# Optimization experiments

Measured on AMD Instinct MI355X. Metric: run time of the kernel, lower is better.

Reference implementation:

```python
import jax, jax.numpy as jnp
import numpy as np

NUM_GROUPS = 32
EPS = 1e-5


def group_norm(x, weight, bias):
    # x: [B, C, H, W]; normalize per (group, sample) over channels-in-group and spatial dims
    B, C, H, W = x.shape
    g = x.reshape(B, NUM_GROUPS, C // NUM_GROUPS, H, W)
    mean = g.mean(axis=(2, 3, 4), keepdims=True)
    var = g.var(axis=(2, 3, 4), keepdims=True)
    g = (g - mean) * jax.lax.rsqrt(var + EPS)
    g = g.reshape(B, C, H, W)
    return g * weight[None, :, None, None] + bias[None, :, None, None]


def conv1x1(x, w, b):
    # x: [B, C, H, W], w: [O, C] (1x1 conv kernel squeezed), b: [O]
    return jnp.einsum('bchw,oc->bohw', x, w) + b[None, :, None, None]


def setup_inputs() -> dict:
    key = jax.random.key(0)
    ks = jax.random.split(key, 6)
    B, C, H, W = 16, 512, 64, 64
    scale = 1.0 / np.sqrt(C)
    x = jax.random.normal(ks[0], (B, C, H, W), dtype=jnp.float32)
    return {
        'x': x,
        'gn_weight': jnp.ones((C,), jnp.float32),
        'gn_bias': jnp.zeros((C,), jnp.float32),
        'wq': jax.random.normal(ks[1], (C, C), jnp.float32) * scale,
        'bq': jnp.zeros((C,), jnp.float32),
        'wk': jax.random.normal(ks[2], (C, C), jnp.float32) * scale,
        'bk': jnp.zeros((C,), jnp.float32),
        'wv': jax.random.normal(ks[3], (C, C), jnp.float32) * scale,
        'bv': jnp.zeros((C,), jnp.float32),
        'wo': jax.random.normal(ks[4], (C, C), jnp.float32) * (scale * 1e-5),
        'bo': jnp.zeros((C,), jnp.float32),
    }


def reference(x, gn_weight, gn_bias, wq, bq, wk, bk, wv, bv, wo, bo):
    B, C, H, W = x.shape
    h = group_norm(x, gn_weight, gn_bias)
    q = conv1x1(h, wq, bq)  # [B, C, H, W]
    k = conv1x1(h, wk, bk)
    v = conv1x1(h, wv, bv)
    q = q.transpose(0, 2, 3, 1).reshape(B, H * W, C)   # [B, HW, C]
    kf = k.reshape(B, C, H * W)                        # [B, C, HW]
    w = jnp.einsum('bnc,bcm->bnm', q, kf) * (C ** -0.5)  # [B, HW, HW]
    w = jax.nn.softmax(w, axis=-1)
    vf = v.transpose(0, 2, 3, 1).reshape(B, H * W, C)
    h = jnp.einsum('bnm,bmc->bnc', w, vf)              # [B, HW, C]
    h = h.reshape(B, H, W, C).transpose(0, 3, 1, 2)    # [B, C, H, W]
    h = conv1x1(h, wo, bo)
    return x + h
```

## Files before the change

### kernel.cpp

```cpp
#include <hip/hip_runtime.h>
#include <stdint.h>

typedef __bf16 bf16x8 __attribute__((ext_vector_type(8)));
typedef float  f32x4  __attribute__((ext_vector_type(4)));
typedef unsigned short ushortx8 __attribute__((ext_vector_type(8)));
typedef unsigned short ushortx4 __attribute__((ext_vector_type(4)));

#define DEVI __device__ __forceinline__

DEVI unsigned short f2bf(float f) {
  union { float f; unsigned int u; } v; v.f = f;
  unsigned int r = v.u + 0x7fffu + ((v.u >> 16) & 1u);
  return (unsigned short)(r >> 16);
}
DEVI float bf2f(unsigned short h) {
  union { unsigned int u; float f; } v; v.u = ((unsigned int)h) << 16;
  return v.f;
}

DEVI void gl_lds16(const unsigned short* g, unsigned short* l) {
  __builtin_amdgcn_global_load_lds(
      (__attribute__((address_space(1))) unsigned int*)g,
      (__attribute__((address_space(3))) unsigned int*)l,
      16, 0, 0);
}

DEVI void raw_barrier() {
  __builtin_amdgcn_sched_barrier(0);
  __builtin_amdgcn_s_barrier();
  __builtin_amdgcn_sched_barrier(0);
}
DEVI void wait_vm4()   { __builtin_amdgcn_s_waitcnt(0x0F74); __builtin_amdgcn_sched_barrier(0); }
DEVI void wait_vm0()   { __builtin_amdgcn_s_waitcnt(0x0F70); __builtin_amdgcn_sched_barrier(0); }
DEVI void wait_lgkm0() { __builtin_amdgcn_s_waitcnt(0xC07F); __builtin_amdgcn_sched_barrier(0); }

DEVI void store_out(float* p, float v) { *p = v; }
DEVI void store_out(unsigned short* p, float v) { *p = f2bf(v); }

__global__ __launch_bounds__(256) void gn_stats(const float* __restrict__ x,
                                                float* __restrict__ stats) {
  const int bg = blockIdx.x;
  const float* p = x + (size_t)bg * 65536;
  const int tid = threadIdx.x;
  float s = 0.f, ss = 0.f;
#pragma unroll 4
  for (int i = 0; i < 64; ++i) {
    float4 v = *(const float4*)(p + (((size_t)i * 256 + tid) << 2));
    s  += v.x + v.y + v.z + v.w;
    ss += v.x * v.x + v.y * v.y + v.z * v.z + v.w * v.w;
  }
  for (int off = 32; off; off >>= 1) { s += __shfl_xor(s, off); ss += __shfl_xor(ss, off); }
  __shared__ float rs[4], rss[4];
  const int lane = tid & 63, wave = tid >> 6;
  if (lane == 0) { rs[wave] = s; rss[wave] = ss; }
  __syncthreads();
  if (tid == 0) {
    float S1 = rs[0] + rs[1] + rs[2] + rs[3];
    float S2 = rss[0] + rss[1] + rss[2] + rss[3];
    float mean = S1 * (1.f / 65536.f);
    float var  = S2 * (1.f / 65536.f) - mean * mean;
    stats[bg * 2 + 0] = mean;
    stats[bg * 2 + 1] = rsqrtf(var + 1e-5f);
  }
}

__global__ __launch_bounds__(256) void gn_apply(const float* __restrict__ x,
                                                const float* __restrict__ stats,
                                                const float* __restrict__ gamma,
                                                const float* __restrict__ beta,
                                                unsigned short* __restrict__ h_t) {
  __shared__ alignas(16) unsigned short tile[64 * 136];
  const int tid = threadIdx.x;
  const int t0 = blockIdx.x * 64;
  const int c0 = blockIdx.y * 128;
  const int b  = blockIdx.z;
  const float* xb = x + ((size_t)b * 512 + c0) * 4096 + t0;
#pragma unroll
  for (int j = 0; j < 8; ++j) {
    int f = tid + j * 256;
    int r = f >> 4;
    int tc = (f & 15) << 2;
    float4 v = *(const float4*)(xb + (size_t)r * 4096 + tc);
    int ch = c0 + r;
    int g = ch >> 4;
    float mean = stats[((size_t)b * 32 + g) * 2 + 0];
    float rstd = stats[((size_t)b * 32 + g) * 2 + 1];
    float ga = gamma[ch] * rstd;
    float be = beta[ch] - mean * ga;
    tile[(tc + 0) * 136 + r] = f2bf(v.x * ga + be);
    tile[(tc + 1) * 136 + r] = f2bf(v.y * ga + be);
    tile[(tc + 2) * 136 + r] = f2bf(v.z * ga + be);
    tile[(tc + 3) * 136 + r] = f2bf(v.w * ga + be);
  }
  __syncthreads();
  unsigned short* hb = h_t + (size_t)b * 4096 * 512;
#pragma unroll
  for (int j = 0; j < 4; ++j) {
    int f = tid + j * 256;
    int tok = f >> 4;
    int cc = (f & 15) << 3;
    ushortx8 v = *(const ushortx8*)&tile[tok * 136 + cc];
    *(ushortx8*)(hb + (size_t)(t0 + tok) * 512 + c0 + cc) = v;
  }
}

__global__ __launch_bounds__(256) void cvt_f32_bf16(const float* __restrict__ s,
                                                    unsigned short* __restrict__ d) {
  int i = (blockIdx.x * 256 + threadIdx.x) * 4;
  float4 v = *(const float4*)(s + i);
  ushortx4 o;
  o[0] = f2bf(v.x); o[1] = f2bf(v.y); o[2] = f2bf(v.z); o[3] = f2bf(v.w);
  *(ushortx4*)(d + i) = o;
}

template <int BIAS_MODE, int RESID, typename OT>
__global__ __launch_bounds__(512, 2) void gemm_nt_256(
    const unsigned short* __restrict__ A, const unsigned short* __restrict__ B,
    OT* __restrict__ D, const float* __restrict__ bias,
    const float* __restrict__ resid, int M, int N, int K,
    long long sA, long long sB, long long sD, long long sR, float alpha) {
  __shared__ alignas(128) char sm[131072];
  char* const sA0 = sm;
  char* const sB0 = sm + 32768;
  char* const sA1 = sm + 65536;
  char* const sB1 = sm + 98304;

  const int tid = threadIdx.x;
  const int bz = blockIdx.x, bn = blockIdx.y, bm = blockIdx.z;
  const unsigned short* Ab = A + (size_t)bz * sA + (size_t)bm * 256 * K;
  const unsigned short* Bb = B + (size_t)bz * sB + (size_t)bn * 256 * K;

  const int lane = tid & 63;
  const int ln = lane & 15, quad = lane >> 4;
  const int wave = tid >> 6;
  const int wm = wave >> 2, wn = wave & 3;

  const int prow = tid >> 3;
  const unsigned ks = (unsigned)((tid & 7) ^ (prow & 7));
  const unsigned srcoff = (unsigned)prow * (unsigned)K + ks * 8u;
  const unsigned ldst = (unsigned)tid * 16u;

  const int aro = (wm * 128 + ln) * 128;
  const int bro = (wn * 64 + ln) * 128;
  const int sl0 = ((quad ^ (ln & 7)) << 4);
  const int sl1 = (((4 + quad) ^ (ln & 7)) << 4);

  f32x4 acc[8][4] = {};
  bf16x8 a0[8], a1[8], b0[4], b1[4];

#define STAGE(G, SMp, h, ktv) do {                                                   \
    const unsigned short* _g = (G) + (unsigned)(h) * 128u * (unsigned)K +            \
                               (unsigned)(ktv) * 64u + srcoff;                       \
    gl_lds16(_g, (unsigned short*)((SMp) + (h) * 16384 + ldst));                     \
    gl_lds16(_g + (size_t)64 * K, (unsigned short*)((SMp) + (h) * 16384 + 8192 + ldst)); \
  } while (0)

#define RD_A(SMp, SL, dst) do { _Pragma("unroll")                                    \
    for (int _mf = 0; _mf < 8; ++_mf)                                                \
      dst[_mf] = *(const bf16x8*)((SMp) + aro + _mf * 2048 + (SL)); } while (0)
#define RD_B(SMp, SL, dst) do { _Pragma("unroll")                                    \
    for (int _nf = 0; _nf < 4; ++_nf)                                                \
      dst[_nf] = *(const bf16x8*)((SMp) + bro + _nf * 2048 + (SL)); } while (0)

#define MM(AF, BF, N0) do {                                                          \
    __builtin_amdgcn_s_setprio(1);                                                   \
    _Pragma("unroll")                                                                \
    for (int _mf = 0; _mf < 8; ++_mf) {                                              \
      acc[_mf][(N0)]     = __builtin_amdgcn_mfma_f32_16x16x32_bf16(AF[_mf], BF[(N0)],     acc[_mf][(N0)],     0, 0, 0); \
      acc[_mf][(N0) + 1] = __builtin_amdgcn_mfma_f32_16x16x32_bf16(AF[_mf], BF[(N0) + 1], acc[_mf][(N0) + 1], 0, 0, 0); \
    }                                                                                \
    __builtin_amdgcn_s_setprio(0);                                                   \
  } while (0)

  STAGE(Ab, sA0, 0, 0); STAGE(Ab, sA0, 1, 0);
  STAGE(Bb, sB0, 0, 0); STAGE(Bb, sB0, 1, 0);
  STAGE(Ab, sA1, 0, 1); STAGE(Ab, sA1, 1, 1);
  wait_vm4();
  raw_barrier();

  const int NI = K >> 7;
  int kt0 = 0;
  for (int i = 0; i < NI - 1; ++i, kt0 += 2) {
    RD_A(sA0, sl0, a0); RD_B(sB0, sl0, b0);
    STAGE(Bb, sB1, 0, kt0 + 1);
    raw_barrier();
    MM(a0, b0, 0);
    raw_barrier();
    RD_A(sA0, sl1, a1); RD_B(sB0, sl1, b1);
    STAGE(Bb, sB1, 1, kt0 + 1);
    raw_barrier();
    MM(a0, b0, 2);
    wait_lgkm0();
    raw_barrier();
    STAGE(Ab, sA0, 0, kt0 + 2);
    raw_barrier();
    MM(a1, b1, 0);
    raw_barrier();
    STAGE(Ab, sA0, 1, kt0 + 2);
    raw_barrier();
    MM(a1, b1, 2);
    wait_vm4();
    raw_barrier();
    RD_A(sA1, sl0, a0); RD_B(sB1, sl0, b0);
    STAGE(Bb, sB0, 0, kt0 + 2);
    raw_barrier();
    MM(a0, b0, 0);
    raw_barrier();
    RD_A(sA1, sl1, a1); RD_B(sB1, sl1, b1);
    STAGE(Bb, sB0, 1, kt0 + 2);
    raw_barrier();
    MM(a0, b0, 2);
    wait_lgkm0();
    raw_barrier();
    STAGE(Ab, sA1, 0, kt0 + 3);
    raw_barrier();
    MM(a1, b1, 0);
    raw_barrier();
    STAGE(Ab, sA1, 1, kt0 + 3);
    raw_barrier();
    MM(a1, b1, 2);
    wait_vm4();
    raw_barrier();
  }
  {
    RD_A(sA0, sl0, a0); RD_B(sB0, sl0, b0);
    STAGE(Bb, sB1, 0, kt0 + 1);
    raw_barrier();
    MM(a0, b0, 0);
    raw_barrier();
    RD_A(sA0, sl1, a1); RD_B(sB0, sl1, b1);
    STAGE(Bb, sB1, 1, kt0 + 1);
    raw_barrier();
    MM(a0, b0, 2);
    MM(a1, b1, 0);
    MM(a1, b1, 2);
    wait_vm0();
    raw_barrier();
    RD_A(sA1, sl0, a0); RD_B(sB1, sl0, b0);
    RD_A(sA1, sl1, a1); RD_B(sB1, sl1, b1);
    MM(a0, b0, 0);
    MM(a0, b0, 2);
    MM(a1, b1, 0);
    MM(a1, b1, 2);
  }
#undef STAGE
#undef RD_A
#undef RD_B
#undef MM

  OT* Db = D + (size_t)bz * sD;
  const float* Rb = RESID ? (resid + (size_t)bz * sR) : nullptr;
#pragma unroll
  for (int mf = 0; mf < 8; ++mf) {
#pragma unroll
    for (int nf = 0; nf < 4; ++nf) {
#pragma unroll
      for (int r = 0; r < 4; ++r) {
        int row = bm * 256 + wm * 128 + mf * 16 + quad * 4 + r;
        int col = bn * 256 + wn * 64 + nf * 16 + ln;
        float v = acc[mf][nf][r] * alpha;
        if (BIAS_MODE == 1) v += bias[row];
        if (BIAS_MODE == 2) v += bias[col];
        size_t idx = (size_t)row * N + col;
        if (RESID) v += Rb[idx];
        store_out(&Db[idx], v);
      }
    }
  }
}

__global__ __launch_bounds__(256) void softmax_rows(unsigned short* __restrict__ S) {
  const int tid = threadIdx.x;
  unsigned short* p = S + (size_t)blockIdx.x * 4096 + tid * 16;
  ushortx8 u0 = *(const ushortx8*)p;
  ushortx8 u1 = *(const ushortx8*)(p + 8);
  float v[16];
#pragma unroll
  for (int i = 0; i < 8; ++i) { v[i] = bf2f(u0[i]); v[i + 8] = bf2f(u1[i]); }
  float m = v[0];
#pragma unroll
  for (int i = 1; i < 16; ++i) m = fmaxf(m, v[i]);
  for (int off = 32; off; off >>= 1) m = fmaxf(m, __shfl_xor(m, off));
  __shared__ float red[4];
  __shared__ float red2[4];
  const int lane = tid & 63, wave = tid >> 6;
  if (lane == 0) red[wave] = m;
  __syncthreads();
  m = fmaxf(fmaxf(red[0], red[1]), fmaxf(red[2], red[3]));
  float s = 0.f;
#pragma unroll
  for (int i = 0; i < 16; ++i) { v[i] = __expf(v[i] - m); s += v[i]; }
  for (int off = 32; off; off >>= 1) s += __shfl_xor(s, off);
  if (lane == 0) red2[wave] = s;
  __syncthreads();
  s = red2[0] + red2[1] + red2[2] + red2[3];
  float inv = 1.f / s;
#pragma unroll
  for (int i = 0; i < 8; ++i) { u0[i] = f2bf(v[i] * inv); u1[i] = f2bf(v[i + 8] * inv); }
  *(ushortx8*)p = u0;
  *(ushortx8*)(p + 8) = u1;
}

extern "C" void kernel_launch(void* const* d_in, const int* in_sizes, int n_in,
                              void* d_out, int out_size, void* d_ws, size_t ws_size,
                              hipStream_t stream) {
  const float* x   = (const float*)d_in[0];
  const float* gnw = (const float*)d_in[1];
  const float* gnb = (const float*)d_in[2];
  const float* wq  = (const float*)d_in[3];
  const float* bq  = (const float*)d_in[4];
  const float* wk  = (const float*)d_in[5];
  const float* bk  = (const float*)d_in[6];
  const float* wv  = (const float*)d_in[7];
  const float* bv  = (const float*)d_in[8];
  const float* wo  = (const float*)d_in[9];
  const float* bo  = (const float*)d_in[10];
  float* out = (float*)d_out;

  const size_t EB = 2097152;

  char* base = (char*)d_ws;
  unsigned short* h_t  = (unsigned short*)base;
  unsigned short* wqb  = (unsigned short*)(base + 67108864);
  unsigned short* wkb  = wqb + 262144;
  unsigned short* wvb  = wkb + 262144;
  unsigned short* wob  = wvb + 262144;
  float*          stats = (float*)(base + 69206016);
  char*           dyn   = base + 69210112;
  size_t rem = ws_size > 69210112 ? ws_size - 69210112 : 0;

  int nb = 1;
  if      (rem >= (size_t)16 * 46137344) nb = 16;
  else if (rem >= (size_t)8  * 46137344) nb = 8;
  else if (rem >= (size_t)4  * 46137344) nb = 4;
  else if (rem >= (size_t)2  * 46137344) nb = 2;

  unsigned short* q  = (unsigned short*)dyn;
  unsigned short* kb = q  + (size_t)nb * EB;
  unsigned short* vb = kb + (size_t)nb * EB;
  unsigned short* Sb = (unsigned short*)(dyn + (size_t)nb * 3 * 4194304);
  unsigned short* attn = q;

  gn_stats<<<512, 256, 0, stream>>>(x, stats);
  gn_apply<<<dim3(64, 4, 16), 256, 0, stream>>>(x, stats, gnw, gnb, h_t);
  cvt_f32_bf16<<<256, 256, 0, stream>>>(wq, wqb);
  cvt_f32_bf16<<<256, 256, 0, stream>>>(wk, wkb);
  cvt_f32_bf16<<<256, 256, 0, stream>>>(wv, wvb);
  cvt_f32_bf16<<<256, 256, 0, stream>>>(wo, wob);

  const float sm_scale = 0.044194173824159216f;

  for (int b0 = 0; b0 < 16; b0 += nb) {
    const unsigned short* hc = h_t + (size_t)b0 * EB;
    gemm_nt_256<2, 0, unsigned short><<<dim3(nb, 2, 16), 512, 0, stream>>>(
        hc, wqb, q, bq, nullptr, 4096, 512, 512, (long long)EB, 0, (long long)EB, 0, 1.f);
    gemm_nt_256<2, 0, unsigned short><<<dim3(nb, 2, 16), 512, 0, stream>>>(
        hc, wkb, kb, bk, nullptr, 4096, 512, 512, (long long)EB, 0, (long long)EB, 0, 1.f);
    gemm_nt_256<1, 0, unsigned short><<<dim3(nb, 16, 2), 512, 0, stream>>>(
        wvb, hc, vb, bv, nullptr, 512, 4096, 512, 0, (long long)EB, (long long)EB, 0, 1.f);
    gemm_nt_256<0, 0, unsigned short><<<dim3(nb, 16, 16), 512, 0, stream>>>(
        q, kb, Sb, nullptr, nullptr, 4096, 4096, 512,
        (long long)EB, (long long)EB, 16777216LL, 0, sm_scale);
    softmax_rows<<<nb * 4096, 256, 0, stream>>>(Sb);
    gemm_nt_256<0, 0, unsigned short><<<dim3(nb, 2, 16), 512, 0, stream>>>(
        Sb, vb, attn, nullptr, nullptr, 4096, 512, 4096,
        16777216LL, (long long)EB, (long long)EB, 0, 1.f);
    gemm_nt_256<1, 1, float><<<dim3(nb, 16, 2), 512, 0, stream>>>(
        wob, attn, out + (size_t)b0 * EB, bo, x + (size_t)b0 * EB,
        512, 4096, 512, 0, (long long)EB, (long long)EB, (long long)EB, 1.f);
  }
}
```

Baseline: 1.242 ms.

## Rewrite GEMM main loop with inline-asm LDS reads and finer waitcnt pipelining

Restructures the bf16 MFMA GEMM main loop so LDS fragment reads for the next sub-step are issued before the current MFMA block, with partial lgkmcnt/vmcnt waits written in inline assembly instead of full drains. Precomputed LDS byte addresses and ds_read_b128 with immediate offsets replace compiler-generated reads, and the staging order is changed so B tiles for two k-steps are prefetched first. The loop now runs uniformly over all iterations, clamping out-of-range tile indices, which removes the separate epilogue but issues redundant loads at the tail. This tries to hide LDS and global latency behind MFMA work. The risk is that hand-set wait counts and asm volatile ordering can be wrong or hamper compiler scheduling.

New measurement: 1.524 ms. 22.7% more time.

```diff
diff --git a/kernel.cpp b/kernel.cpp
--- a/kernel.cpp
+++ b/kernel.cpp
@@ -25,14 +25,17 @@
       16, 0, 0);
 }
 
-DEVI void raw_barrier() {
+DEVI unsigned lds_off(const void* p) {
+  return (unsigned)(unsigned long long)(__attribute__((address_space(3))) const char*)(const char*)p;
+}
+
+DEVI void abar() {
   __builtin_amdgcn_sched_barrier(0);
-  __builtin_amdgcn_s_barrier();
+  asm volatile("s_barrier");
   __builtin_amdgcn_sched_barrier(0);
 }
-DEVI void wait_vm4()   { __builtin_amdgcn_s_waitcnt(0x0F74); __builtin_amdgcn_sched_barrier(0); }
-DEVI void wait_vm0()   { __builtin_amdgcn_s_waitcnt(0x0F70); __builtin_amdgcn_sched_barrier(0); }
-DEVI void wait_lgkm0() { __builtin_amdgcn_s_waitcnt(0xC07F); __builtin_amdgcn_sched_barrier(0); }
+#define AWT_VM(N)   do { asm volatile("s_waitcnt vmcnt(" #N ")");   __builtin_amdgcn_sched_barrier(0); } while (0)
+#define AWT_LGKM(N) do { asm volatile("s_waitcnt lgkmcnt(" #N ")"); __builtin_amdgcn_sched_barrier(0); } while (0)
 
 DEVI void store_out(float* p, float v) { *p = v; }
 DEVI void store_out(unsigned short* p, float v) { *p = f2bf(v); }
@@ -145,6 +148,16 @@
   const int sl0 = ((quad ^ (ln & 7)) << 4);
   const int sl1 = (((4 + quad) ^ (ln & 7)) << 4);
 
+  const unsigned base = lds_off(sm);
+  const unsigned aA0s0 = base + 0u     + (unsigned)aro + (unsigned)sl0;
+  const unsigned aA0s1 = base + 0u     + (unsigned)aro + (unsigned)sl1;
+  const unsigned aB0s0 = base + 32768u + (unsigned)bro + (unsigned)sl0;
+  const unsigned aB0s1 = base + 32768u + (unsigned)bro + (unsigned)sl1;
+  const unsigned aA1s0 = base + 65536u + (unsigned)aro + (unsigned)sl0;
+  const unsigned aA1s1 = base + 65536u + (unsigned)aro + (unsigned)sl1;
+  const unsigned aB1s0 = base + 98304u + (unsigned)bro + (unsigned)sl0;
+  const unsigned aB1s1 = base + 98304u + (unsigned)bro + (unsigned)sl1;
+
   f32x4 acc[8][4] = {};
   bf16x8 a0[8], a1[8], b0[4], b1[4];
 
@@ -155,12 +168,23 @@
     gl_lds16(_g + (size_t)64 * K, (unsigned short*)((SMp) + (h) * 16384 + 8192 + ldst)); \
   } while (0)
 
-#define RD_A(SMp, SL, dst) do { _Pragma("unroll")                                    \
-    for (int _mf = 0; _mf < 8; ++_mf)                                                \
-      dst[_mf] = *(const bf16x8*)((SMp) + aro + _mf * 2048 + (SL)); } while (0)
-#define RD_B(SMp, SL, dst) do { _Pragma("unroll")                                    \
-    for (int _nf = 0; _nf < 4; ++_nf)                                                \
-      dst[_nf] = *(const bf16x8*)((SMp) + bro + _nf * 2048 + (SL)); } while (0)
+#define RD_A8(dst, ad) do {                                                          \
+    asm volatile("ds_read_b128 %0, %1 offset:0"     : "=v"(dst[0]) : "v"(ad));       \
+    asm volatile("ds_read_b128 %0, %1 offset:2048"  : "=v"(dst[1]) : "v"(ad));       \
+    asm volatile("ds_read_b128 %0, %1 offset:4096"  : "=v"(dst[2]) : "v"(ad));       \
+    asm volatile("ds_read_b128 %0, %1 offset:6144"  : "=v"(dst[3]) : "v"(ad));       \
+    asm volatile("ds_read_b128 %0, %1 offset:8192"  : "=v"(dst[4]) : "v"(ad));       \
+    asm volatile("ds_read_b128 %0, %1 offset:10240" : "=v"(dst[5]) : "v"(ad));       \
+    asm volatile("ds_read_b128 %0, %1 offset:12288" : "=v"(dst[6]) : "v"(ad));       \
+    asm volatile("ds_read_b128 %0, %1 offset:14336" : "=v"(dst[7]) : "v"(ad));       \
+  } while (0)
+
+#define RD_B4(dst, ad) do {                                                          \
+    asm volatile("ds_read_b128 %0, %1 offset:0"     : "=v"(dst[0]) : "v"(ad));       \
+    asm volatile("ds_read_b128 %0, %1 offset:2048"  : "=v"(dst[1]) : "v"(ad));       \
+    asm volatile("ds_read_b128 %0, %1 offset:4096"  : "=v"(dst[2]) : "v"(ad));       \
+    asm volatile("ds_read_b128 %0, %1 offset:6144"  : "=v"(dst[3]) : "v"(ad));       \
+  } while (0)
 
 #define MM(AF, BF, N0) do {                                                          \
     __builtin_amdgcn_s_setprio(1);                                                   \
@@ -172,80 +196,69 @@
     __builtin_amdgcn_s_setprio(0);                                                   \
   } while (0)
 
+  const int KT = K >> 6;
+  const int NI = K >> 7;
+
   STAGE(Ab, sA0, 0, 0); STAGE(Ab, sA0, 1, 0);
   STAGE(Bb, sB0, 0, 0); STAGE(Bb, sB0, 1, 0);
-  STAGE(Ab, sA1, 0, 1); STAGE(Ab, sA1, 1, 1);
-  wait_vm4();
-  raw_barrier();
-
-  const int NI = K >> 7;
-  int kt0 = 0;
-  for (int i = 0; i < NI - 1; ++i, kt0 += 2) {
-    RD_A(sA0, sl0, a0); RD_B(sB0, sl0, b0);
-    STAGE(Bb, sB1, 0, kt0 + 1);
-    raw_barrier();
+  STAGE(Bb, sB1, 0, 1); STAGE(Bb, sB1, 1, 1);
+  AWT_VM(4);
+  abar();
+  RD_B4(b0, aB0s0);
+  RD_A8(a0, aA0s0);
+
+  for (int i = 0; i < NI; ++i) {
+    const int kt1 = 2 * i + 1;
+    const int kt2 = (2 * i + 2 < KT) ? 2 * i + 2 : KT - 1;
+    const int kt3 = (2 * i + 3 < KT) ? 2 * i + 3 : KT - 1;
+    RD_B4(b1, aB0s1);
+    STAGE(Ab, sA1, 0, kt1);
+    abar(); AWT_LGKM(4);
     MM(a0, b0, 0);
-    raw_barrier();
-    RD_A(sA0, sl1, a1); RD_B(sB0, sl1, b1);
-    STAGE(Bb, sB1, 1, kt0 + 1);
-    raw_barrier();
+    abar();
+    RD_A8(a1, aA0s1);
+    STAGE(Ab, sA1, 1, kt1);
+    abar(); AWT_LGKM(8);
     MM(a0, b0, 2);
-    wait_lgkm0();
-    raw_barrier();
-    STAGE(Ab, sA0, 0, kt0 + 2);
-    raw_barrier();
+    AWT_VM(4);
+    abar();
+    RD_B4(b0, aB1s0);
+    STAGE(Bb, sB0, 0, kt2);
+    abar(); AWT_LGKM(4);
     MM(a1, b1, 0);
-    raw_barrier();
-    STAGE(Ab, sA0, 1, kt0 + 2);
-    raw_barrier();
+    AWT_VM(2);
+    abar();
+    RD_A8(a0, aA1s0);
+    STAGE(Bb, sB0, 1, kt2);
+    abar(); AWT_LGKM(8);
     MM(a1, b1, 2);
-    wait_vm4();
-    raw_barrier();
-    RD_A(sA1, sl0, a0); RD_B(sB1, sl0, b0);
-    STAGE(Bb, sB0, 0, kt0 + 2);
-    raw_barrier();
+    abar();
+    RD_B4(b1, aB1s1);
+    STAGE(Ab, sA0, 0, kt2);
+    abar(); AWT_LGKM(4);
     MM(a0, b0, 0);
-    raw_barrier();
-    RD_A(sA1, sl1, a1); RD_B(sB1, sl1, b1);
-    STAGE(Bb, sB0, 1, kt0 + 2);
-    raw_barrier();
+    abar();
+    RD_A8(a1, aA1s1);
+    STAGE(Ab, sA0, 1, kt2);
+    abar(); AWT_LGKM(8);
     MM(a0, b0, 2);
-    wait_lgkm0();
-    raw_barrier();
-    STAGE(Ab, sA1, 0, kt0 + 3);
-    raw_barrier();
+    AWT_VM(4);
+    abar();
+    RD_B4(b0, aB0s0);
+    STAGE(Bb, sB1, 0, kt3);
+    abar(); AWT_LGKM(4);
     MM(a1, b1, 0);
-    raw_barrier();
-    STAGE(Ab, sA1, 1, kt0 + 3);
-    raw_barrier();
+    AWT_VM(2);
+    abar();
+    RD_A8(a0, aA0s0);
+    STAGE(Bb, sB1, 1, kt3);
+    abar(); AWT_LGKM(8);
     MM(a1, b1, 2);
-    wait_vm4();
-    raw_barrier();
-  }
-  {
-    RD_A(sA0, sl0, a0); RD_B(sB0, sl0, b0);
-    STAGE(Bb, sB1, 0, kt0 + 1);
-    raw_barrier();
-    MM(a0, b0, 0);
-    raw_barrier();
-    RD_A(sA0, sl1, a1); RD_B(sB0, sl1, b1);
-    STAGE(Bb, sB1, 1, kt0 + 1);
-    raw_barrier();
-    MM(a0, b0, 2);
-    MM(a1, b1, 0);
-    MM(a1, b1, 2);
-    wait_vm0();
-    raw_barrier();
-    RD_A(sA1, sl0, a0); RD_B(sB1, sl0, b0);
-    RD_A(sA1, sl1, a1); RD_B(sB1, sl1, b1);
-    MM(a0, b0, 0);
-    MM(a0, b0, 2);
-    MM(a1, b1, 0);
-    MM(a1, b1, 2);
+    abar();
   }
 #undef STAGE
-#undef RD_A
-#undef RD_B
+#undef RD_A8
+#undef RD_B4
 #undef MM
 
   OT* Db = D + (size_t)bz * sD;
```

## Restructure GEMM mainloop into quadrant ping-pong schedule and remap QK^T block grid

Applied to the files above, without the earlier changes.

Rewrites the GEMM main loop so LDS fragment reads and MFMAs work on quarter tiles (4x2 fragments with both K halves). Global-to-LDS staging now loads full 256-row tiles per stage, with explicit inline-asm waitcnts and barriers interleaved between MFMA groups, aiming to overlap LDS reads, global loads and matrix math more evenly. The score GEMM also gets a grid remap that puts the batch on z and walks N tiles within an M row, for better L2 reuse of Q tiles. Risks: the inline waitcnt accounting and the clamped tail stage indices are fragile and could introduce races or redundant loads.

After: 2.782 ms. +124.0%, slower.

```diff
diff --git a/kernel.cpp b/kernel.cpp
--- a/kernel.cpp
+++ b/kernel.cpp
@@ -25,14 +25,8 @@
       16, 0, 0);
 }
 
-DEVI void raw_barrier() {
-  __builtin_amdgcn_sched_barrier(0);
-  __builtin_amdgcn_s_barrier();
-  __builtin_amdgcn_sched_barrier(0);
-}
-DEVI void wait_vm4()   { __builtin_amdgcn_s_waitcnt(0x0F74); __builtin_amdgcn_sched_barrier(0); }
-DEVI void wait_vm0()   { __builtin_amdgcn_s_waitcnt(0x0F70); __builtin_amdgcn_sched_barrier(0); }
-DEVI void wait_lgkm0() { __builtin_amdgcn_s_waitcnt(0xC07F); __builtin_amdgcn_sched_barrier(0); }
+#define AWT_VM(N)   asm volatile("s_waitcnt vmcnt(" #N ")")
+#define AWT_LGKM(N) asm volatile("s_waitcnt lgkmcnt(" #N ")")
 
 DEVI void store_out(float* p, float v) { *p = v; }
 DEVI void store_out(unsigned short* p, float v) { *p = f2bf(v); }
@@ -113,7 +107,7 @@
   *(ushortx4*)(d + i) = o;
 }
 
-template <int BIAS_MODE, int RESID, typename OT>
+template <int BIAS_MODE, int RESID, int REMAP, typename OT>
 __global__ __launch_bounds__(512, 2) void gemm_nt_256(
     const unsigned short* __restrict__ A, const unsigned short* __restrict__ B,
     OT* __restrict__ D, const float* __restrict__ bias,
@@ -126,7 +120,14 @@
   char* const sB1 = sm + 98304;
 
   const int tid = threadIdx.x;
-  const int bz = blockIdx.x, bn = blockIdx.y, bm = blockIdx.z;
+  int bz, bn, bm;
+  if (REMAP) {
+    bz = blockIdx.z;
+    bm = (int)blockIdx.y >> 1;
+    bn = ((int)blockIdx.y & 1) * 8 + (int)blockIdx.x;
+  } else {
+    bz = blockIdx.x; bn = blockIdx.y; bm = blockIdx.z;
+  }
   const unsigned short* Ab = A + (size_t)bz * sA + (size_t)bm * 256 * K;
   const unsigned short* Bb = B + (size_t)bz * sB + (size_t)bn * 256 * K;
 
@@ -146,107 +147,102 @@
   const int sl1 = (((4 + quad) ^ (ln & 7)) << 4);
 
   f32x4 acc[8][4] = {};
-  bf16x8 a0[8], a1[8], b0[4], b1[4];
-
-#define STAGE(G, SMp, h, ktv) do {                                                   \
-    const unsigned short* _g = (G) + (unsigned)(h) * 128u * (unsigned)K +            \
-                               (unsigned)(ktv) * 64u + srcoff;                       \
-    gl_lds16(_g, (unsigned short*)((SMp) + (h) * 16384 + ldst));                     \
-    gl_lds16(_g + (size_t)64 * K, (unsigned short*)((SMp) + (h) * 16384 + 8192 + ldst)); \
+  bf16x8 aL0[8], aL1[8], aH[8], bL[4], bH[4];
+
+#define STAGE4(G, SMp, ktv) do {                                                     \
+    const unsigned short* _g = (G) + (unsigned)(ktv) * 64u + srcoff;                 \
+    gl_lds16(_g,                   (unsigned short*)((SMp) + ldst));                 \
+    gl_lds16(_g + (size_t)64 * K,  (unsigned short*)((SMp) + 8192 + ldst));          \
+    gl_lds16(_g + (size_t)128 * K, (unsigned short*)((SMp) + 16384 + ldst));         \
+    gl_lds16(_g + (size_t)192 * K, (unsigned short*)((SMp) + 24576 + ldst));         \
   } while (0)
 
-#define RD_A(SMp, SL, dst) do { _Pragma("unroll")                                    \
-    for (int _mf = 0; _mf < 8; ++_mf)                                                \
-      dst[_mf] = *(const bf16x8*)((SMp) + aro + _mf * 2048 + (SL)); } while (0)
-#define RD_B(SMp, SL, dst) do { _Pragma("unroll")                                    \
-    for (int _nf = 0; _nf < 4; ++_nf)                                                \
-      dst[_nf] = *(const bf16x8*)((SMp) + bro + _nf * 2048 + (SL)); } while (0)
-
-#define MM(AF, BF, N0) do {                                                          \
+#define RD_AQ(dst, SMp, MF0) do { _Pragma("unroll")                                  \
+    for (int _mi = 0; _mi < 4; ++_mi) {                                              \
+      dst[_mi * 2 + 0] = *(const bf16x8*)((SMp) + aro + (MF0 + _mi) * 2048 + sl0);   \
+      dst[_mi * 2 + 1] = *(const bf16x8*)((SMp) + aro + (MF0 + _mi) * 2048 + sl1);   \
+    } } while (0)
+#define RD_BQ(dst, SMp, NF0) do { _Pragma("unroll")                                  \
+    for (int _ni = 0; _ni < 2; ++_ni) {                                              \
+      dst[_ni * 2 + 0] = *(const bf16x8*)((SMp) + bro + (NF0 + _ni) * 2048 + sl0);   \
+      dst[_ni * 2 + 1] = *(const bf16x8*)((SMp) + bro + (NF0 + _ni) * 2048 + sl1);   \
+    } } while (0)
+
+#define MMQ(AQ, BQ, MF0, NF0) do {                                                   \
     __builtin_amdgcn_s_setprio(1);                                                   \
     _Pragma("unroll")                                                                \
-    for (int _mf = 0; _mf < 8; ++_mf) {                                              \
-      acc[_mf][(N0)]     = __builtin_amdgcn_mfma_f32_16x16x32_bf16(AF[_mf], BF[(N0)],     acc[_mf][(N0)],     0, 0, 0); \
-      acc[_mf][(N0) + 1] = __builtin_amdgcn_mfma_f32_16x16x32_bf16(AF[_mf], BF[(N0) + 1], acc[_mf][(N0) + 1], 0, 0, 0); \
+    for (int _mi = 0; _mi < 4; ++_mi) {                                              \
+      _Pragma("unroll")                                                              \
+      for (int _ni = 0; _ni < 2; ++_ni) {                                            \
+        f32x4 _c = acc[(MF0) + _mi][(NF0) + _ni];                                    \
+        _c = __builtin_amdgcn_mfma_f32_16x16x32_bf16(AQ[_mi * 2 + 0], BQ[_ni * 2 + 0], _c, 0, 0, 0); \
+        _c = __builtin_amdgcn_mfma_f32_16x16x32_bf16(AQ[_mi * 2 + 1], BQ[_ni * 2 + 1], _c, 0, 0, 0); \
+        acc[(MF0) + _mi][(NF0) + _ni] = _c;                                          \
+      }                                                                              \
     }                                                                                \
     __builtin_amdgcn_s_setprio(0);                                                   \
   } while (0)
 
-  STAGE(Ab, sA0, 0, 0); STAGE(Ab, sA0, 1, 0);
-  STAGE(Bb, sB0, 0, 0); STAGE(Bb, sB0, 1, 0);
-  STAGE(Ab, sA1, 0, 1); STAGE(Ab, sA1, 1, 1);
-  wait_vm4();
-  raw_barrier();
-
+  const int KT = K >> 6;
   const int NI = K >> 7;
-  int kt0 = 0;
-  for (int i = 0; i < NI - 1; ++i, kt0 += 2) {
-    RD_A(sA0, sl0, a0); RD_B(sB0, sl0, b0);
-    STAGE(Bb, sB1, 0, kt0 + 1);
-    raw_barrier();
-    MM(a0, b0, 0);
-    raw_barrier();
-    RD_A(sA0, sl1, a1); RD_B(sB0, sl1, b1);
-    STAGE(Bb, sB1, 1, kt0 + 1);
-    raw_barrier();
-    MM(a0, b0, 2);
-    wait_lgkm0();
-    raw_barrier();
-    STAGE(Ab, sA0, 0, kt0 + 2);
-    raw_barrier();
-    MM(a1, b1, 0);
-    raw_barrier();
-    STAGE(Ab, sA0, 1, kt0 + 2);
-    raw_barrier();
-    MM(a1, b1, 2);
-    wait_vm4();
-    raw_barrier();
-    RD_A(sA1, sl0, a0); RD_B(sB1, sl0, b0);
-    STAGE(Bb, sB0, 0, kt0 + 2);
-    raw_barrier();
-    MM(a0, b0, 0);
-    raw_barrier();
-    RD_A(sA1, sl1, a1); RD_B(sB1, sl1, b1);
-    STAGE(Bb, sB0, 1, kt0 + 2);
-    raw_barrier();
-    MM(a0, b0, 2);
-    wait_lgkm0();
-    raw_barrier();
-    STAGE(Ab, sA1, 0, kt0 + 3);
-    raw_barrier();
-    MM(a1, b1, 0);
-    raw_barrier();
-    STAGE(Ab, sA1, 1, kt0 + 3);
-    raw_barrier();
-    MM(a1, b1, 2);
-    wait_vm4();
-    raw_barrier();
-  }
-  {
-    RD_A(sA0, sl0, a0); RD_B(sB0, sl0, b0);
-    STAGE(Bb, sB1, 0, kt0 + 1);
-    raw_barrier();
-    MM(a0, b0, 0);
-    raw_barrier();
-    RD_A(sA0, sl1, a1); RD_B(sB0, sl1, b1);
-    STAGE(Bb, sB1, 1, kt0 + 1);
-    raw_barrier();
-    MM(a0, b0, 2);
-    MM(a1, b1, 0);
-    MM(a1, b1, 2);
-    wait_vm0();
-    raw_barrier();
-    RD_A(sA1, sl0, a0); RD_B(sB1, sl0, b0);
-    RD_A(sA1, sl1, a1); RD_B(sB1, sl1, b1);
-    MM(a0, b0, 0);
-    MM(a0, b0, 2);
-    MM(a1, b1, 0);
-    MM(a1, b1, 2);
-  }
-#undef STAGE
-#undef RD_A
-#undef RD_B
-#undef MM
+
+  STAGE4(Ab, sA0, 0);
+  STAGE4(Bb, sB0, 0);
+  STAGE4(Ab, sA1, 1);
+  AWT_VM(4);
+  __builtin_amdgcn_s_barrier();
+  RD_AQ(aL0, sA0, 0);
+  RD_BQ(bL,  sB0, 0);
+
+  for (int i = 0; i < NI; ++i) {
+    const int t1 = 2 * i + 1;
+    const int t2 = (2 * i + 2 < KT) ? 2 * i + 2 : KT - 1;
+    const int t3 = (2 * i + 3 < KT) ? 2 * i + 3 : KT - 1;
+    RD_AQ(aH, sA0, 4);
+    STAGE4(Bb, sB1, t1);
+    __builtin_amdgcn_s_barrier(); AWT_LGKM(0);
+    MMQ(aL0, bL, 0, 0);
+    __builtin_amdgcn_s_barrier();
+    RD_BQ(bH, sB0, 2);
+    AWT_VM(4);
+    __builtin_amdgcn_s_barrier(); AWT_LGKM(0);
+    MMQ(aH, bL, 4, 0);
+    __builtin_amdgcn_s_barrier();
+    RD_AQ(aL1, sA1, 0);
+    STAGE4(Ab, sA0, t2);
+    AWT_VM(4);
+    __builtin_amdgcn_s_barrier(); AWT_LGKM(0);
+    MMQ(aH, bH, 4, 2);
+    __builtin_amdgcn_s_barrier();
+    RD_BQ(bL, sB1, 0);
+    __builtin_amdgcn_s_barrier(); AWT_LGKM(0);
+    MMQ(aL0, bH, 0, 2);
+    __builtin_amdgcn_s_barrier();
+    RD_AQ(aH, sA1, 4);
+    STAGE4(Bb, sB0, t2);
+    __builtin_amdgcn_s_barrier(); AWT_LGKM(0);
+    MMQ(aL1, bL, 0, 0);
+    __builtin_amdgcn_s_barrier();
+    RD_BQ(bH, sB1, 2);
+    AWT_VM(4);
+    __builtin_amdgcn_s_barrier(); AWT_LGKM(0);
+    MMQ(aH, bL, 4, 0);
+    __builtin_amdgcn_s_barrier();
+    RD_AQ(aL0, sA0, 0);
+    STAGE4(Ab, sA1, t3);
+    AWT_VM(4);
+    __builtin_amdgcn_s_barrier(); AWT_LGKM(0);
+    MMQ(aH, bH, 4, 2);
+    __builtin_amdgcn_s_barrier();
+    RD_BQ(bL, sB0, 0);
+    __builtin_amdgcn_s_barrier(); AWT_LGKM(0);
+    MMQ(aL1, bH, 0, 2);
+    __builtin_amdgcn_s_barrier();
+  }
+#undef STAGE4
+#undef RD_AQ
+#undef RD_BQ
+#undef MMQ
 
   OT* Db = D + (size_t)bz * sD;
   const float* Rb = RESID ? (resid + (size_t)bz * sR) : nullptr;
@@ -352,20 +348,20 @@
 
   for (int b0 = 0; b0 < 16; b0 += nb) {
     const unsigned short* hc = h_t + (size_t)b0 * EB;
-    gemm_nt_256<2, 0, unsigned short><<<dim3(nb, 2, 16), 512, 0, stream>>>(
+    gemm_nt_256<2, 0, 0, unsigned short><<<dim3(nb, 2, 16), 512, 0, stream>>>(
         hc, wqb, q, bq, nullptr, 4096, 512, 512, (long long)EB, 0, (long long)EB, 0, 1.f);
-    gemm_nt_256<2, 0, unsigned short><<<dim3(nb, 2, 16), 512, 0, stream>>>(
+    gemm_nt_256<2, 0, 0, unsigned short><<<dim3(nb, 2, 16), 512, 0, stream>>>(
         hc, wkb, kb, bk, nullptr, 4096, 512, 512, (long long)EB, 0, (long long)EB, 0, 1.f);
-    gemm_nt_256<1, 0, unsigned short><<<dim3(nb, 16, 2), 512, 0, stream>>>(
+    gemm_nt_256<1, 0, 0, unsigned short><<<dim3(nb, 16, 2), 512, 0, stream>>>(
         wvb, hc, vb, bv, nullptr, 512, 4096, 512, 0, (long long)EB, (long long)EB, 0, 1.f);
-    gemm_nt_256<0, 0, unsigned short><<<dim3(nb, 16, 16), 512, 0, stream>>>(
+    gemm_nt_256<0, 0, 1, unsigned short><<<dim3(8, 32, nb), 512, 0, stream>>>(
         q, kb, Sb, nullptr, nullptr, 4096, 4096, 512,
         (long long)EB, (long long)EB, 16777216LL, 0, sm_scale);
     softmax_rows<<<nb * 4096, 256, 0, stream>>>(Sb);
-    gemm_nt_256<0, 0, unsigned short><<<dim3(nb, 2, 16), 512, 0, stream>>>(
+    gemm_nt_256<0, 0, 0, unsigned short><<<dim3(nb, 2, 16), 512, 0, stream>>>(
         Sb, vb, attn, nullptr, nullptr, 4096, 512, 4096,
         16777216LL, (long long)EB, (long long)EB, 0, 1.f);
-    gemm_nt_256<1, 1, float><<<dim3(nb, 16, 2), 512, 0, stream>>>(
+    gemm_nt_256<1, 1, 0, float><<<dim3(nb, 16, 2), 512, 0, stream>>>(
         wob, attn, out + (size_t)b0 * EB, bo, x + (size_t)b0 * EB,
         512, 4096, 512, 0, (long long)EB, (long long)EB, (long long)EB, 1.f);
   }
```
